# Kernel optimization log

Measured on AMD Instinct MI355X. Metric: run time of the kernel, lower is better.

Reference implementation:

```python
import jax, jax.numpy as jnp
import numpy as np

B, N = 128, 1369
DINO, CLIP, H = 384, 512, 8
D = CLIP // H  # head_dim = 64
EPS = 1e-5


def setup_inputs() -> dict:
    key = jax.random.key(0)
    ks = jax.random.split(key, 8)
    s_clip = 1.0 / np.sqrt(CLIP)
    s_dino = 1.0 / np.sqrt(DINO)
    return {
        "dino_features": jax.random.normal(ks[0], (B, N, DINO), jnp.float32),
        "clip_features": jax.random.normal(ks[1], (B, CLIP), jnp.float32),
        "Wq": jax.random.uniform(ks[2], (CLIP, CLIP), jnp.float32, -s_clip, s_clip),
        "bq": jnp.zeros((CLIP,), jnp.float32),
        "Wk": jax.random.uniform(ks[3], (DINO, CLIP), jnp.float32, -s_dino, s_dino),
        "bk": jnp.zeros((CLIP,), jnp.float32),
        "Wv": jax.random.uniform(ks[4], (DINO, CLIP), jnp.float32, -s_dino, s_dino),
        "bv": jnp.zeros((CLIP,), jnp.float32),
        "temperature": jnp.ones((1,), jnp.float32),
        "ln_gamma": jnp.ones((CLIP,), jnp.float32),
        "ln_beta": jnp.zeros((CLIP,), jnp.float32),
    }


def reference(dino_features, clip_features, Wq, bq, Wk, bk, Wv, bv,
              temperature, ln_gamma, ln_beta):
    # Q: (B, H, D) -- single query token from CLIP
    Q = (clip_features @ Wq + bq).reshape(B, H, D)
    # K, V: (B, N, H, D)
    K = (dino_features @ Wk + bk).reshape(B, N, H, D)
    V = (dino_features @ Wv + bv).reshape(B, N, H, D)
    scale = jnp.sqrt(jnp.float32(D)) * temperature[0]
    # attention logits over patches: (B, H, N)
    logits = jnp.einsum("bhd,bnhd->bhn", Q, K) / scale
    attn = jax.nn.softmax(logits, axis=-1)  # dropout is identity in eval mode
    out = jnp.einsum("bhn,bnhd->bhd", attn, V).reshape(B, CLIP)
    # LayerNorm over last dim
    mu = out.mean(axis=-1, keepdims=True)
    var = out.var(axis=-1, keepdims=True)
    return (out - mu) * jax.lax.rsqrt(var + EPS) * ln_gamma + ln_beta
```

## Files before the change

### kernel.cpp

```cpp
#include <hip/hip_runtime.h>
#include <math.h>

#define B_    128
#define N_    1369
#define DINO_ 384
#define CLIP_ 512
#define H_    8
#define CHUNKS 6
#define CH     229

__device__ __forceinline__ float wave_sum(float v) {
  v += __shfl_xor(v, 1);  v += __shfl_xor(v, 2);  v += __shfl_xor(v, 4);
  v += __shfl_xor(v, 8);  v += __shfl_xor(v, 16); v += __shfl_xor(v, 32);
  return v;
}

__device__ __forceinline__ float fold8(const float* v, int lane) {
  float a0, a1, a2, a3;
  {
    float t0 = __shfl_xor(v[0], 32), t1 = __shfl_xor(v[1], 32);
    float t2 = __shfl_xor(v[2], 32), t3 = __shfl_xor(v[3], 32);
    float u0 = __shfl_xor(v[4], 32), u1 = __shfl_xor(v[5], 32);
    float u2 = __shfl_xor(v[6], 32), u3 = __shfl_xor(v[7], 32);
    const bool hi = (lane & 32) != 0;
    a0 = hi ? v[4] + u0 : v[0] + t0;
    a1 = hi ? v[5] + u1 : v[1] + t1;
    a2 = hi ? v[6] + u2 : v[2] + t2;
    a3 = hi ? v[7] + u3 : v[3] + t3;
  }
  float b0, b1;
  {
    float t0 = __shfl_xor(a0, 16), t1 = __shfl_xor(a1, 16);
    float t2 = __shfl_xor(a2, 16), t3 = __shfl_xor(a3, 16);
    const bool hi = (lane & 16) != 0;
    b0 = hi ? a2 + t2 : a0 + t0;
    b1 = hi ? a3 + t3 : a1 + t1;
  }
  float c0;
  {
    float t0 = __shfl_xor(b0, 8), t1 = __shfl_xor(b1, 8);
    const bool hi = (lane & 8) != 0;
    c0 = hi ? b1 + t1 : b0 + t0;
  }
  c0 += __shfl_xor(c0, 4);
  c0 += __shfl_xor(c0, 2);
  c0 += __shfl_xor(c0, 1);
  return c0;
}

__device__ __forceinline__ void bcast8(float p, float* P) {
  P[0] = p;
  P[1] = __shfl_xor(P[0], 8);
  P[2] = __shfl_xor(P[0], 16);
  P[3] = __shfl_xor(P[1], 16);
  P[4] = __shfl_xor(P[0], 32);
  P[5] = __shfl_xor(P[1], 32);
  P[6] = __shfl_xor(P[2], 32);
  P[7] = __shfl_xor(P[3], 32);
}

__global__ __launch_bounds__(256) void kq(const float* __restrict__ clip,
                                          const float* __restrict__ Wq,
                                          const float* __restrict__ bq,
                                          float* __restrict__ Q) {
  const int b = blockIdx.x;
  const int c = blockIdx.y * 256 + threadIdx.x;
  __shared__ float cl[CLIP_];
  cl[threadIdx.x] = clip[b * CLIP_ + threadIdx.x];
  cl[threadIdx.x + 256] = clip[b * CLIP_ + threadIdx.x + 256];
  __syncthreads();
  float acc = bq[c];
  #pragma unroll 8
  for (int j = 0; j < CLIP_; ++j) acc += cl[j] * Wq[j * CLIP_ + c];
  Q[b * CLIP_ + c] = acc;
}

__global__ __launch_bounds__(256) void kt(const float* __restrict__ Wk,
                                          float* __restrict__ WkT) {
  __shared__ float tile[64][65];
  const int tx = threadIdx.x & 63, ty = threadIdx.x >> 6;
  const int c0 = blockIdx.x * 64, j0 = blockIdx.y * 64;
  #pragma unroll
  for (int k = 0; k < 16; ++k) {
    const int jj = ty + 4 * k;
    tile[jj][tx] = Wk[(j0 + jj) * CLIP_ + c0 + tx];
  }
  __syncthreads();
  #pragma unroll
  for (int k = 0; k < 16; ++k) {
    const int cc = ty + 4 * k;
    WkT[(size_t)(c0 + cc) * DINO_ + j0 + tx] = tile[tx][cc];
  }
}

__global__ __launch_bounds__(256) void kqk(const float* __restrict__ WkT,
                                           const float* __restrict__ Q,
                                           const float* __restrict__ temp,
                                           float* __restrict__ qkout) {
  const int b = blockIdx.x;
  const int e = blockIdx.y * 256 + threadIdx.x;
  __shared__ float qs[CLIP_];
  qs[threadIdx.x] = Q[b * CLIP_ + threadIdx.x];
  qs[threadIdx.x + 256] = Q[b * CLIP_ + threadIdx.x + 256];
  __syncthreads();
  const int h = e / DINO_;
  const int j = e - h * DINO_;
  const float rs = 1.0f / (8.0f * temp[0]);
  float acc = 0.0f;
  #pragma unroll 8
  for (int d = 0; d < 64; ++d)
    acc += WkT[(size_t)(h * 64 + d) * DINO_ + j] * qs[h * 64 + d];
  qkout[(size_t)b * 3072 + e] = acc * rs;
}

__global__ __launch_bounds__(256, 3) void kmain(const float* __restrict__ dino,
                                                const float* __restrict__ qk,
                                                float* __restrict__ ps,
                                                float* __restrict__ pl) {
  const int blk = blockIdx.x;
  const int b = blk / CHUNKS;
  const int c = blk - b * CHUNKS;
  const int n0 = c * CH;
  const int n1 = min(N_, n0 + CH);
  const int tid = threadIdx.x, w = tid >> 6, lane = tid & 63;
  const int phi = (((lane >> 5) & 1) << 2) | (((lane >> 4) & 1) << 1) | ((lane >> 3) & 1);

  float qr[H_][6];
  const float* qkb = qk + (size_t)b * 3072;
  #pragma unroll
  for (int h = 0; h < H_; ++h)
    #pragma unroll
    for (int i = 0; i < 3; ++i) {
      const float2 t = *(const float2*)(qkb + h * DINO_ + i * 128 + 2 * lane);
      qr[h][2 * i] = t.x;  qr[h][2 * i + 1] = t.y;
    }

  float s[H_][6];
  float l = 0.0f;
  #pragma unroll
  for (int j = 0; j < H_; ++j)
    #pragma unroll
    for (int k = 0; k < 6; ++k) s[j][k] = 0.0f;

  const float* dbase = dino + (size_t)b * N_ * DINO_;

  for (int n = n0 + w; n < n1; n += 8) {
    const int n2 = n + 4;
    const bool hb = n2 < n1;
    const float* ra = dbase + (size_t)n * DINO_;
    const float* rb = dbase + (size_t)(hb ? n2 : n) * DINO_;
    float2 xa[3], xb[3];
    #pragma unroll
    for (int i = 0; i < 3; ++i) xa[i] = *(const float2*)(ra + i * 128 + 2 * lane);
    #pragma unroll
    for (int i = 0; i < 3; ++i) xb[i] = *(const float2*)(rb + i * 128 + 2 * lane);

    float va[H_];
    #pragma unroll
    for (int h = 0; h < H_; ++h)
      va[h] = qr[h][0] * xa[0].x + qr[h][1] * xa[0].y + qr[h][2] * xa[1].x
            + qr[h][3] * xa[1].y + qr[h][4] * xa[2].x + qr[h][5] * xa[2].y;
    float vb[H_];
    #pragma unroll
    for (int h = 0; h < H_; ++h)
      vb[h] = qr[h][0] * xb[0].x + qr[h][1] * xb[0].y + qr[h][2] * xb[1].x
            + qr[h][3] * xb[1].y + qr[h][4] * xb[2].x + qr[h][5] * xb[2].y;

    const float pa = __expf(fold8(va, lane));
    const float pb = __expf(fold8(vb, lane));
    float Pa[H_], Pb[H_];
    bcast8(pa, Pa);
    bcast8(pb, Pb);

    l += pa;
    #pragma unroll
    for (int j = 0; j < H_; ++j) {
      s[j][0] += Pa[j] * xa[0].x;  s[j][1] += Pa[j] * xa[0].y;
      s[j][2] += Pa[j] * xa[1].x;  s[j][3] += Pa[j] * xa[1].y;
      s[j][4] += Pa[j] * xa[2].x;  s[j][5] += Pa[j] * xa[2].y;
    }
    if (hb) {
      l += pb;
      #pragma unroll
      for (int j = 0; j < H_; ++j) {
        s[j][0] += Pb[j] * xb[0].x;  s[j][1] += Pb[j] * xb[0].y;
        s[j][2] += Pb[j] * xb[1].x;  s[j][3] += Pb[j] * xb[1].y;
        s[j][4] += Pb[j] * xb[2].x;  s[j][5] += Pb[j] * xb[2].y;
      }
    }
  }

  __shared__ float sm[2][3072];
  __shared__ float lm[2][H_];
  if (w >= 2) {
    #pragma unroll
    for (int j = 0; j < H_; ++j)
      #pragma unroll
      for (int k = 0; k < 6; ++k)
        sm[w - 2][(phi ^ j) * DINO_ + (k >> 1) * 128 + 2 * lane + (k & 1)] = s[j][k];
    if ((lane & 7) == 0) lm[w - 2][phi] = l;
  }
  __syncthreads();
  if (w < 2) {
    #pragma unroll
    for (int j = 0; j < H_; ++j)
      #pragma unroll
      for (int k = 0; k < 6; ++k)
        s[j][k] += sm[w][(phi ^ j) * DINO_ + (k >> 1) * 128 + 2 * lane + (k & 1)];
    if ((lane & 7) == 0) l += lm[w][phi];
  }
  __syncthreads();
  if (w == 1) {
    #pragma unroll
    for (int j = 0; j < H_; ++j)
      #pragma unroll
      for (int k = 0; k < 6; ++k)
        sm[0][(phi ^ j) * DINO_ + (k >> 1) * 128 + 2 * lane + (k & 1)] = s[j][k];
    if ((lane & 7) == 0) lm[0][phi] = l;
  }
  __syncthreads();
  if (w == 0) {
    #pragma unroll
    for (int j = 0; j < H_; ++j)
      #pragma unroll
      for (int k = 0; k < 6; ++k)
        s[j][k] += sm[0][(phi ^ j) * DINO_ + (k >> 1) * 128 + 2 * lane + (k & 1)];
    if ((lane & 7) == 0) l += lm[0][phi];
    float* pso = ps + (size_t)blk * 3072;
    #pragma unroll
    for (int j = 0; j < H_; ++j)
      #pragma unroll
      for (int k = 0; k < 6; ++k)
        pso[(phi ^ j) * DINO_ + (k >> 1) * 128 + 2 * lane + (k & 1)] = s[j][k];
    if ((lane & 7) == 0) pl[blk * H_ + phi] = l;
  }
}

__global__ __launch_bounds__(256) void km(const float* __restrict__ ps,
                                          const float* __restrict__ pl,
                                          float* __restrict__ sf) {
  const int b = blockIdx.x, tid = threadIdx.x;
  __shared__ float rL[H_];
  if (tid < H_) {
    float L = 0.0f;
    #pragma unroll
    for (int cc = 0; cc < CHUNKS; ++cc) L += pl[(b * CHUNKS + cc) * H_ + tid];
    rL[tid] = 1.0f / L;
  }
  __syncthreads();
  #pragma unroll
  for (int r = 0; r < 12; ++r) {
    const int e = tid + 256 * r;
    float acc = 0.0f;
    #pragma unroll
    for (int cc = 0; cc < CHUNKS; ++cc)
      acc += ps[(size_t)(b * CHUNKS + cc) * 3072 + e];
    sf[(size_t)b * 3072 + e] = acc * rL[e / DINO_];
  }
}

__global__ __launch_bounds__(512) void kf(const float* __restrict__ sf,
                                          const float* __restrict__ Wv,
                                          const float* __restrict__ bv,
                                          const float* __restrict__ gamma,
                                          const float* __restrict__ beta,
                                          float* __restrict__ out) {
  const int b = blockIdx.x, tid = threadIdx.x;
  const int w = tid >> 6, lane = tid & 63;
  __shared__ float sfl[3072];
  #pragma unroll
  for (int k = 0; k < 6; ++k) sfl[tid + 512 * k] = sf[(size_t)b * 3072 + tid + 512 * k];
  __syncthreads();
  const float* srow = sfl + (tid >> 6) * DINO_;
  float acc = bv[tid];
  #pragma unroll 8
  for (int d = 0; d < DINO_; ++d) acc += srow[d] * Wv[d * CLIP_ + tid];
  float sum = wave_sum(acc);
  float sq  = wave_sum(acc * acc);
  __shared__ float rS[8], rQ[8];
  if (lane == 0) { rS[w] = sum; rQ[w] = sq; }
  __syncthreads();
  float tot = 0.0f, totq = 0.0f;
  #pragma unroll
  for (int i = 0; i < 8; ++i) { tot += rS[i]; totq += rQ[i]; }
  const float mu = tot * (1.0f / 512.0f);
  const float var = totq * (1.0f / 512.0f) - mu * mu;
  const float rstd = rsqrtf(var + 1e-5f);
  out[(size_t)b * CLIP_ + tid] = (acc - mu) * rstd * gamma[tid] + beta[tid];
}

extern "C" void kernel_launch(void* const* d_in, const int* in_sizes, int n_in,
                              void* d_out, int out_size, void* d_ws, size_t ws_size,
                              hipStream_t stream) {
  const float* dino  = (const float*)d_in[0];
  const float* clip  = (const float*)d_in[1];
  const float* Wq    = (const float*)d_in[2];
  const float* bq    = (const float*)d_in[3];
  const float* Wk    = (const float*)d_in[4];
  const float* Wv    = (const float*)d_in[6];
  const float* bv    = (const float*)d_in[7];
  const float* temp  = (const float*)d_in[8];
  const float* gamma = (const float*)d_in[9];
  const float* beta  = (const float*)d_in[10];
  float* out = (float*)d_out;

  float* ws  = (float*)d_ws;
  float* Q   = ws;
  float* WkT = Q   + 65536;
  float* qk  = WkT + 196608;
  float* ps  = qk  + 393216;
  float* pl  = ps  + 2359296;
  float* sf  = pl  + 6144;

  kq  <<<dim3(B_, 2),  256, 0, stream>>>(clip, Wq, bq, Q);
  kt  <<<dim3(8, 6),   256, 0, stream>>>(Wk, WkT);
  kqk <<<dim3(B_, 12), 256, 0, stream>>>(WkT, Q, temp, qk);
  kmain<<<B_ * CHUNKS, 256, 0, stream>>>(dino, qk, ps, pl);
  km  <<<B_,           256, 0, stream>>>(ps, pl, sf);
  kf  <<<B_,           512, 0, stream>>>(sf, Wv, bv, gamma, beta, out);
}
```

Baseline: 469.2 us.

## Remap kmain lanes to per-head slices, drop transpose, fuse merge with output

The main attention kernel now assigns 8 lanes per head. Each lane owns 48 contiguous feature elements loaded as float4, so the per-row logit needs only a 3-step shuffle reduction and the fold/broadcast shuffle trees go away. The kernel processes one row per wave per iteration instead of two, with 48 accumulators. The Wk transpose kernel is removed by having kqk read Wk rows directly with float4 loads. The chunk-merge kernel is fused into the final Wv/LayerNorm kernel, which removes two launches and the sf round trip. The costs are more register pressure from the 48-wide accumulators and less row-level ILP, plus strided Wk reads in kqk.

```diff
diff --git a/kernel.cpp b/kernel.cpp
--- a/kernel.cpp
+++ b/kernel.cpp
@@ -8,55 +8,12 @@
 #define H_    8
 #define CHUNKS 6
 #define CH     229
+#define SMP    52
 
 __device__ __forceinline__ float wave_sum(float v) {
   v += __shfl_xor(v, 1);  v += __shfl_xor(v, 2);  v += __shfl_xor(v, 4);
   v += __shfl_xor(v, 8);  v += __shfl_xor(v, 16); v += __shfl_xor(v, 32);
   return v;
-}
-
-__device__ __forceinline__ float fold8(const float* v, int lane) {
-  float a0, a1, a2, a3;
-  {
-    float t0 = __shfl_xor(v[0], 32), t1 = __shfl_xor(v[1], 32);
-    float t2 = __shfl_xor(v[2], 32), t3 = __shfl_xor(v[3], 32);
-    float u0 = __shfl_xor(v[4], 32), u1 = __shfl_xor(v[5], 32);
-    float u2 = __shfl_xor(v[6], 32), u3 = __shfl_xor(v[7], 32);
-    const bool hi = (lane & 32) != 0;
-    a0 = hi ? v[4] + u0 : v[0] + t0;
-    a1 = hi ? v[5] + u1 : v[1] + t1;
-    a2 = hi ? v[6] + u2 : v[2] + t2;
-    a3 = hi ? v[7] + u3 : v[3] + t3;
-  }
-  float b0, b1;
-  {
-    float t0 = __shfl_xor(a0, 16), t1 = __shfl_xor(a1, 16);
-    float t2 = __shfl_xor(a2, 16), t3 = __shfl_xor(a3, 16);
-    const bool hi = (lane & 16) != 0;
-    b0 = hi ? a2 + t2 : a0 + t0;
-    b1 = hi ? a3 + t3 : a1 + t1;
-  }
-  float c0;
-  {
-    float t0 = __shfl_xor(b0, 8), t1 = __shfl_xor(b1, 8);
-    const bool hi = (lane & 8) != 0;
-    c0 = hi ? b1 + t1 : b0 + t0;
-  }
-  c0 += __shfl_xor(c0, 4);
-  c0 += __shfl_xor(c0, 2);
-  c0 += __shfl_xor(c0, 1);
-  return c0;
-}
-
-__device__ __forceinline__ void bcast8(float p, float* P) {
-  P[0] = p;
-  P[1] = __shfl_xor(P[0], 8);
-  P[2] = __shfl_xor(P[0], 16);
-  P[3] = __shfl_xor(P[1], 16);
-  P[4] = __shfl_xor(P[0], 32);
-  P[5] = __shfl_xor(P[1], 32);
-  P[6] = __shfl_xor(P[2], 32);
-  P[7] = __shfl_xor(P[3], 32);
 }
 
 __global__ __launch_bounds__(256) void kq(const float* __restrict__ clip,
@@ -75,25 +32,7 @@
   Q[b * CLIP_ + c] = acc;
 }
 
-__global__ __launch_bounds__(256) void kt(const float* __restrict__ Wk,
-                                          float* __restrict__ WkT) {
-  __shared__ float tile[64][65];
-  const int tx = threadIdx.x & 63, ty = threadIdx.x >> 6;
-  const int c0 = blockIdx.x * 64, j0 = blockIdx.y * 64;
-  #pragma unroll
-  for (int k = 0; k < 16; ++k) {
-    const int jj = ty + 4 * k;
-    tile[jj][tx] = Wk[(j0 + jj) * CLIP_ + c0 + tx];
-  }
-  __syncthreads();
-  #pragma unroll
-  for (int k = 0; k < 16; ++k) {
-    const int cc = ty + 4 * k;
-    WkT[(size_t)(c0 + cc) * DINO_ + j0 + tx] = tile[tx][cc];
-  }
-}
-
-__global__ __launch_bounds__(256) void kqk(const float* __restrict__ WkT,
+__global__ __launch_bounds__(256) void kqk(const float* __restrict__ Wk,
                                            const float* __restrict__ Q,
                                            const float* __restrict__ temp,
                                            float* __restrict__ qkout) {
@@ -106,11 +45,17 @@
   const int h = e / DINO_;
   const int j = e - h * DINO_;
   const float rs = 1.0f / (8.0f * temp[0]);
-  float acc = 0.0f;
-  #pragma unroll 8
-  for (int d = 0; d < 64; ++d)
-    acc += WkT[(size_t)(h * 64 + d) * DINO_ + j] * qs[h * 64 + d];
-  qkout[(size_t)b * 3072 + e] = acc * rs;
+  const float* wrow = Wk + (size_t)j * CLIP_ + h * 64;
+  const float* qrow = qs + h * 64;
+  float a0 = 0.f, a1 = 0.f, a2 = 0.f, a3 = 0.f;
+  #pragma unroll
+  for (int d = 0; d < 64; d += 4) {
+    const float4 wv = *(const float4*)(wrow + d);
+    const float4 qv = *(const float4*)(qrow + d);
+    a0 += wv.x * qv.x;  a1 += wv.y * qv.y;
+    a2 += wv.z * qv.z;  a3 += wv.w * qv.w;
+  }
+  qkout[(size_t)b * 3072 + e] = ((a0 + a1) + (a2 + a3)) * rs;
 }
 
 __global__ __launch_bounds__(256, 3) void kmain(const float* __restrict__ dino,
@@ -123,124 +68,119 @@
   const int n0 = c * CH;
   const int n1 = min(N_, n0 + CH);
   const int tid = threadIdx.x, w = tid >> 6, lane = tid & 63;
-  const int phi = (((lane >> 5) & 1) << 2) | (((lane >> 4) & 1) << 1) | ((lane >> 3) & 1);
-
-  float qr[H_][6];
-  const float* qkb = qk + (size_t)b * 3072;
-  #pragma unroll
-  for (int h = 0; h < H_; ++h)
-    #pragma unroll
-    for (int i = 0; i < 3; ++i) {
-      const float2 t = *(const float2*)(qkb + h * DINO_ + i * 128 + 2 * lane);
-      qr[h][2 * i] = t.x;  qr[h][2 * i + 1] = t.y;
-    }
-
-  float s[H_][6];
+  const int h = lane >> 3, sl = lane & 7;
+  const int off = 4 * sl;
+
+  float qr[48];
+  {
+    const float* qb = qk + (size_t)b * 3072 + h * DINO_ + off;
+    #pragma unroll
+    for (int t = 0; t < 12; ++t) {
+      const float4 v = *(const float4*)(qb + 32 * t);
+      qr[4*t] = v.x; qr[4*t+1] = v.y; qr[4*t+2] = v.z; qr[4*t+3] = v.w;
+    }
+  }
+  float s[48];
+  #pragma unroll
+  for (int k = 0; k < 48; ++k) s[k] = 0.0f;
   float l = 0.0f;
-  #pragma unroll
-  for (int j = 0; j < H_; ++j)
-    #pragma unroll
-    for (int k = 0; k < 6; ++k) s[j][k] = 0.0f;
-
-  const float* dbase = dino + (size_t)b * N_ * DINO_;
-
-  for (int n = n0 + w; n < n1; n += 8) {
-    const int n2 = n + 4;
-    const bool hb = n2 < n1;
-    const float* ra = dbase + (size_t)n * DINO_;
-    const float* rb = dbase + (size_t)(hb ? n2 : n) * DINO_;
-    float2 xa[3], xb[3];
-    #pragma unroll
-    for (int i = 0; i < 3; ++i) xa[i] = *(const float2*)(ra + i * 128 + 2 * lane);
-    #pragma unroll
-    for (int i = 0; i < 3; ++i) xb[i] = *(const float2*)(rb + i * 128 + 2 * lane);
-
-    float va[H_];
-    #pragma unroll
-    for (int h = 0; h < H_; ++h)
-      va[h] = qr[h][0] * xa[0].x + qr[h][1] * xa[0].y + qr[h][2] * xa[1].x
-            + qr[h][3] * xa[1].y + qr[h][4] * xa[2].x + qr[h][5] * xa[2].y;
-    float vb[H_];
-    #pragma unroll
-    for (int h = 0; h < H_; ++h)
-      vb[h] = qr[h][0] * xb[0].x + qr[h][1] * xb[0].y + qr[h][2] * xb[1].x
-            + qr[h][3] * xb[1].y + qr[h][4] * xb[2].x + qr[h][5] * xb[2].y;
-
-    const float pa = __expf(fold8(va, lane));
-    const float pb = __expf(fold8(vb, lane));
-    float Pa[H_], Pb[H_];
-    bcast8(pa, Pa);
-    bcast8(pb, Pb);
-
-    l += pa;
-    #pragma unroll
-    for (int j = 0; j < H_; ++j) {
-      s[j][0] += Pa[j] * xa[0].x;  s[j][1] += Pa[j] * xa[0].y;
-      s[j][2] += Pa[j] * xa[1].x;  s[j][3] += Pa[j] * xa[1].y;
-      s[j][4] += Pa[j] * xa[2].x;  s[j][5] += Pa[j] * xa[2].y;
-    }
-    if (hb) {
-      l += pb;
-      #pragma unroll
-      for (int j = 0; j < H_; ++j) {
-        s[j][0] += Pb[j] * xb[0].x;  s[j][1] += Pb[j] * xb[0].y;
-        s[j][2] += Pb[j] * xb[1].x;  s[j][3] += Pb[j] * xb[1].y;
-        s[j][4] += Pb[j] * xb[2].x;  s[j][5] += Pb[j] * xb[2].y;
-      }
-    }
-  }
-
-  __shared__ float sm[2][3072];
+
+  const float* dbase = dino + (size_t)b * N_ * DINO_ + off;
+
+  #pragma unroll 1
+  for (int n = n0 + w; n < n1; n += 4) {
+    const float* row = dbase + (size_t)n * DINO_;
+    float4 x[12];
+    #pragma unroll
+    for (int t = 0; t < 12; ++t) x[t] = *(const float4*)(row + 32 * t);
+
+    float a0 = 0.f, a1 = 0.f, a2 = 0.f, a3 = 0.f;
+    #pragma unroll
+    for (int t = 0; t < 12; ++t) {
+      a0 += qr[4*t]   * x[t].x;
+      a1 += qr[4*t+1] * x[t].y;
+      a2 += qr[4*t+2] * x[t].z;
+      a3 += qr[4*t+3] * x[t].w;
+    }
+    float v = (a0 + a1) + (a2 + a3);
+    v += __shfl_xor(v, 1);
+    v += __shfl_xor(v, 2);
+    v += __shfl_xor(v, 4);
+    const float p = __expf(v);
+    l += p;
+    #pragma unroll
+    for (int t = 0; t < 12; ++t) {
+      s[4*t]   += p * x[t].x;
+      s[4*t+1] += p * x[t].y;
+      s[4*t+2] += p * x[t].z;
+      s[4*t+3] += p * x[t].w;
+    }
+  }
+
+  __shared__ float sm[2][64 * SMP];
   __shared__ float lm[2][H_];
   if (w >= 2) {
-    #pragma unroll
-    for (int j = 0; j < H_; ++j)
-      #pragma unroll
-      for (int k = 0; k < 6; ++k)
-        sm[w - 2][(phi ^ j) * DINO_ + (k >> 1) * 128 + 2 * lane + (k & 1)] = s[j][k];
-    if ((lane & 7) == 0) lm[w - 2][phi] = l;
+    float* dst = &sm[w - 2][lane * SMP];
+    #pragma unroll
+    for (int t = 0; t < 12; ++t)
+      *(float4*)(dst + 4 * t) = make_float4(s[4*t], s[4*t+1], s[4*t+2], s[4*t+3]);
+    if (sl == 0) lm[w - 2][h] = l;
   }
   __syncthreads();
   if (w < 2) {
-    #pragma unroll
-    for (int j = 0; j < H_; ++j)
-      #pragma unroll
-      for (int k = 0; k < 6; ++k)
-        s[j][k] += sm[w][(phi ^ j) * DINO_ + (k >> 1) * 128 + 2 * lane + (k & 1)];
-    if ((lane & 7) == 0) l += lm[w][phi];
+    const float* src = &sm[w][lane * SMP];
+    #pragma unroll
+    for (int t = 0; t < 12; ++t) {
+      const float4 v = *(const float4*)(src + 4 * t);
+      s[4*t] += v.x; s[4*t+1] += v.y; s[4*t+2] += v.z; s[4*t+3] += v.w;
+    }
+    l += lm[w][h];
   }
   __syncthreads();
   if (w == 1) {
-    #pragma unroll
-    for (int j = 0; j < H_; ++j)
-      #pragma unroll
-      for (int k = 0; k < 6; ++k)
-        sm[0][(phi ^ j) * DINO_ + (k >> 1) * 128 + 2 * lane + (k & 1)] = s[j][k];
-    if ((lane & 7) == 0) lm[0][phi] = l;
+    float* dst = &sm[0][lane * SMP];
+    #pragma unroll
+    for (int t = 0; t < 12; ++t)
+      *(float4*)(dst + 4 * t) = make_float4(s[4*t], s[4*t+1], s[4*t+2], s[4*t+3]);
+    if (sl == 0) lm[0][h] = l;
   }
   __syncthreads();
   if (w == 0) {
-    #pragma unroll
-    for (int j = 0; j < H_; ++j)
-      #pragma unroll
-      for (int k = 0; k < 6; ++k)
-        s[j][k] += sm[0][(phi ^ j) * DINO_ + (k >> 1) * 128 + 2 * lane + (k & 1)];
-    if ((lane & 7) == 0) l += lm[0][phi];
-    float* pso = ps + (size_t)blk * 3072;
-    #pragma unroll
-    for (int j = 0; j < H_; ++j)
-      #pragma unroll
-      for (int k = 0; k < 6; ++k)
-        pso[(phi ^ j) * DINO_ + (k >> 1) * 128 + 2 * lane + (k & 1)] = s[j][k];
-    if ((lane & 7) == 0) pl[blk * H_ + phi] = l;
-  }
-}
-
-__global__ __launch_bounds__(256) void km(const float* __restrict__ ps,
-                                          const float* __restrict__ pl,
-                                          float* __restrict__ sf) {
+    const float* src = &sm[0][lane * SMP];
+    #pragma unroll
+    for (int t = 0; t < 12; ++t) {
+      const float4 v = *(const float4*)(src + 4 * t);
+      s[4*t] += v.x; s[4*t+1] += v.y; s[4*t+2] += v.z; s[4*t+3] += v.w;
+    }
+    l += lm[0][h];
+    float* pso = ps + (size_t)blk * 3072 + h * DINO_ + off;
+    #pragma unroll
+    for (int t = 0; t < 12; ++t)
+      *(float4*)(pso + 32 * t) = make_float4(s[4*t], s[4*t+1], s[4*t+2], s[4*t+3]);
+    if (sl == 0) pl[blk * H_ + h] = l;
+  }
+}
+
+__global__ __launch_bounds__(512) void kmf(const float* __restrict__ ps,
+                                           const float* __restrict__ pl,
+                                           const float* __restrict__ Wv,
+                                           const float* __restrict__ bv,
+                                           const float* __restrict__ gamma,
+                                           const float* __restrict__ beta,
+                                           float* __restrict__ out) {
   const int b = blockIdx.x, tid = threadIdx.x;
+  __shared__ float sfl[3072];
   __shared__ float rL[H_];
+  float a[6];
+  #pragma unroll
+  for (int r = 0; r < 6; ++r) {
+    const int e = tid + 512 * r;
+    float acc = 0.0f;
+    #pragma unroll
+    for (int cc = 0; cc < CHUNKS; ++cc)
+      acc += ps[(size_t)(b * CHUNKS + cc) * 3072 + e];
+    a[r] = acc;
+  }
   if (tid < H_) {
     float L = 0.0f;
     #pragma unroll
@@ -249,28 +189,12 @@
   }
   __syncthreads();
   #pragma unroll
-  for (int r = 0; r < 12; ++r) {
-    const int e = tid + 256 * r;
-    float acc = 0.0f;
-    #pragma unroll
-    for (int cc = 0; cc < CHUNKS; ++cc)
-      acc += ps[(size_t)(b * CHUNKS + cc) * 3072 + e];
-    sf[(size_t)b * 3072 + e] = acc * rL[e / DINO_];
-  }
-}
-
-__global__ __launch_bounds__(512) void kf(const float* __restrict__ sf,
-                                          const float* __restrict__ Wv,
-                                          const float* __restrict__ bv,
-                                          const float* __restrict__ gamma,
-                                          const float* __restrict__ beta,
-                                          float* __restrict__ out) {
-  const int b = blockIdx.x, tid = threadIdx.x;
+  for (int r = 0; r < 6; ++r) {
+    const int e = tid + 512 * r;
+    sfl[e] = a[r] * rL[e / DINO_];
+  }
+  __syncthreads();
   const int w = tid >> 6, lane = tid & 63;
-  __shared__ float sfl[3072];
-  #pragma unroll
-  for (int k = 0; k < 6; ++k) sfl[tid + 512 * k] = sf[(size_t)b * 3072 + tid + 512 * k];
-  __syncthreads();
   const float* srow = sfl + (tid >> 6) * DINO_;
   float acc = bv[tid];
   #pragma unroll 8
@@ -306,16 +230,12 @@
 
   float* ws  = (float*)d_ws;
   float* Q   = ws;
-  float* WkT = Q   + 65536;
-  float* qk  = WkT + 196608;
-  float* ps  = qk  + 393216;
+  float* qkb = Q   + 65536;
+  float* ps  = qkb + 393216;
   float* pl  = ps  + 2359296;
-  float* sf  = pl  + 6144;
-
-  kq  <<<dim3(B_, 2),  256, 0, stream>>>(clip, Wq, bq, Q);
-  kt  <<<dim3(8, 6),   256, 0, stream>>>(Wk, WkT);
-  kqk <<<dim3(B_, 12), 256, 0, stream>>>(WkT, Q, temp, qk);
-  kmain<<<B_ * CHUNKS, 256, 0, stream>>>(dino, qk, ps, pl);
-  km  <<<B_,           256, 0, stream>>>(ps, pl, sf);
-  kf  <<<B_,           512, 0, stream>>>(sf, Wv, bv, gamma, beta, out);
-}
+
+  kq   <<<dim3(B_, 2),  256, 0, stream>>>(clip, Wq, bq, Q);
+  kqk  <<<dim3(B_, 12), 256, 0, stream>>>(Wk, Q, temp, qkb);
+  kmain<<<B_ * CHUNKS,  256, 0, stream>>>(dino, qkb, ps, pl);
+  kmf  <<<B_,           512, 0, stream>>>(ps, pl, Wv, bv, gamma, beta, out);
+}
```

New measurement: 537.9 us. +14.6%, slower.
